# Performance work log

Measured on AMD Instinct MI355X. Metric: run time of the kernel, lower is better.

Reference implementation:

```python
import jax, jax.numpy as jnp
import numpy as np

G, B, T = 8, 32, 1000
I_TOT, H_TOT = 512, 512
Ig, Hg = I_TOT // G, H_TOT // G  # 64, 64


def setup_inputs() -> dict:
    key = jax.random.key(0)
    ks = jax.random.split(key, 6)
    return {
        "x_seq": jax.random.normal(ks[0], (B, T, I_TOT), dtype=jnp.float32),
        "h0": jax.random.normal(ks[1], (G, B, Hg), dtype=jnp.float32),
        # per-group GRU params, TF gate order [z, r, n]
        "W": jax.random.normal(ks[2], (G, Ig, 3 * Hg), dtype=jnp.float32) * 0.1,   # kernel
        "U": jax.random.normal(ks[3], (G, Hg, 3 * Hg), dtype=jnp.float32) * 0.1,   # recurrent kernel
        "b_i": jax.random.normal(ks[4], (G, 3 * Hg), dtype=jnp.float32) * 0.1,     # input bias
        "b_h": jax.random.normal(ks[5], (G, 3 * Hg), dtype=jnp.float32) * 0.1,     # recurrent bias
    }


def _grouped_gru(x_seq, h0, W, U, b_i, b_h):
    b, t, _ = x_seq.shape
    g, ig, _ = W.shape
    hg = U.shape[1]
    # [B,T,I] -> [T,G,B,Ig]
    x = x_seq.reshape(b, t, g, ig).transpose(1, 2, 0, 3)

    def step(h, x_t):
        # h: [G,B,Hg], x_t: [G,B,Ig]
        gx = jnp.einsum('gbi,gij->gbj', x_t, W) + b_i[:, None, :]  # [G,B,3Hg]
        gh = jnp.einsum('gbh,ghj->gbj', h, U) + b_h[:, None, :]    # [G,B,3Hg]
        xz, xr, xn = jnp.split(gx, 3, axis=-1)
        hz, hr, hn = jnp.split(gh, 3, axis=-1)
        z = jax.nn.sigmoid(xz + hz)
        r = jax.nn.sigmoid(xr + hr)
        n = jnp.tanh(xn + r * hn)  # reset_after=True: reset applied after recurrent matmul
        h_new = z * h + (1.0 - z) * n
        return h_new, h_new

    h_out, ys = jax.lax.scan(step, h0, x)  # ys: [T,G,B,Hg]
    output = ys.transpose(2, 0, 1, 3).reshape(b, t, g * hg)  # [B,T,H]
    return output, h_out


def reference(x_seq, h0, W, U, b_i, b_h):
    return _grouped_gru(x_seq, h0, W, U, b_i, b_h)
```

## Files before the change

### kernel.cpp

```cpp
#include <hip/hip_runtime.h>

#define TS 1000

typedef _Float16 half2v __attribute__((ext_vector_type(2)));

__device__ __forceinline__ float rl(float v, int l) {
    return __int_as_float(__builtin_amdgcn_readlane(__float_as_int(v), l));
}
__device__ __forceinline__ int rli(int v, int l) {
    return __builtin_amdgcn_readlane(v, l);
}
__device__ __forceinline__ float fsig(float x) {
    return __builtin_amdgcn_rcpf(1.0f + __expf(-x));
}
__device__ __forceinline__ float ftanh(float x) {
    return 1.0f - 2.0f * __builtin_amdgcn_rcpf(1.0f + __expf(2.0f * x));
}

__global__ __launch_bounds__(512)
__attribute__((amdgpu_waves_per_eu(2, 2)))
void gru_win(const float* __restrict__ x, const float* __restrict__ h0,
             const float* __restrict__ W, const float* __restrict__ U,
             const float* __restrict__ bi, const float* __restrict__ bh,
             float* __restrict__ out, float* __restrict__ hout)
{
    __shared__ float4 ppart[2][4][4][64];
    __shared__ float4 psum[2][4][64];

    const int tid  = threadIdx.x;
    const int lane = tid & 63;
    const int wid  = tid >> 6;
    const bool cons = (wid == 0);
    const bool prod = (wid == 1) || (wid == 2) || (wid == 3) || (wid == 5);
    const int sw   = (wid == 5) ? 3 : (wid - 1);
    const int kb   = __builtin_amdgcn_readfirstlane(prod ? sw * 16 : 0);

    const int g = blockIdx.x >> 5, b = blockIdx.x & 31;

    int uw[96];
    float h = 0.f, bhz = 0.f, bhr = 0.f, bhn = 0.f;
    float* op = out + (size_t)b * (TS * 512) + g * 64 + lane;
    if (cons) {
        const float* Ug = U + (size_t)g * (64 * 192) + lane;
        #pragma unroll
        for (int k2 = 0; k2 < 32; ++k2) {
            #pragma unroll
            for (int gate = 0; gate < 3; ++gate) {
                const float a = Ug[(2 * k2) * 192 + gate * 64];
                const float c = Ug[(2 * k2 + 1) * 192 + gate * 64];
                half2v p; p.x = (_Float16)a; p.y = (_Float16)c;
                uw[gate * 32 + k2] = __builtin_bit_cast(int, p);
            }
        }
        #pragma unroll
        for (int k2 = 0; k2 < 32; ++k2)
            asm volatile("" : "+v"(uw[k2]), "+v"(uw[32 + k2]), "+v"(uw[64 + k2]));
        bhz = bh[g * 192 + lane];
        bhr = bh[g * 192 + 64 + lane];
        bhn = bh[g * 192 + 128 + lane];
        h   = h0[(g * 32 + b) * 64 + lane];
    }

    float w0[16], w1[16], w2[16];
    float bz = 0.f, br = 0.f, bn = 0.f;
    const float* xp = x + (size_t)b * (TS * 512) + g * 64 + lane;
    float xa0 = 0, xa1 = 0, xa2 = 0, xa3 = 0, xb0 = 0, xb1 = 0, xb2 = 0, xb3 = 0;
    if (prod) {
        const float* Wg = W + (size_t)g * (64 * 192) + (size_t)kb * 192 + lane;
        #pragma unroll
        for (int k = 0; k < 16; ++k) {
            w0[k] = Wg[k * 192];
            w1[k] = Wg[k * 192 + 64];
            w2[k] = Wg[k * 192 + 128];
        }
        #pragma unroll
        for (int k = 0; k < 16; ++k)
            asm volatile("" : "+v"(w0[k]), "+v"(w1[k]), "+v"(w2[k]));
        if (sw == 0) {
            bz = bi[g * 192 + lane];
            br = bi[g * 192 + 64 + lane];
            bn = bi[g * 192 + 128 + lane];
        }
    }

#define XLOAD(DST, T_)                                                        \
    { const float* pp_ = xp + (size_t)(T_) * 512;                             \
      asm volatile("global_load_dword %0, %1, off" : "=v"(DST) : "v"(pp_)); }

#define PPROD(XS, SLOT, J)                                                    \
    {                                                                         \
        float az = bz, ar = br, an = bn, az2 = 0.f, ar2 = 0.f, an2 = 0.f;     \
        _Pragma("unroll")                                                     \
        for (int k = 0; k < 8; ++k) {                                         \
            const float s = rl(XS, kb + k);                                   \
            az = fmaf(s, w0[k], az); ar = fmaf(s, w1[k], ar); an = fmaf(s, w2[k], an); \
        }                                                                     \
        _Pragma("unroll")                                                     \
        for (int k = 8; k < 16; ++k) {                                        \
            const float s = rl(XS, kb + k);                                   \
            az2 = fmaf(s, w0[k], az2); ar2 = fmaf(s, w1[k], ar2); an2 = fmaf(s, w2[k], an2); \
        }                                                                     \
        ppart[SLOT][J][sw][lane] = make_float4(az + az2, ar + ar2, an + an2, 0.f); \
    }

#define PREDUCE(SLOT)                                                         \
    {                                                                         \
        const float4 q0 = ppart[SLOT][sw][0][lane];                           \
        const float4 q1 = ppart[SLOT][sw][1][lane];                           \
        const float4 q2 = ppart[SLOT][sw][2][lane];                           \
        const float4 q3 = ppart[SLOT][sw][3][lane];                           \
        psum[SLOT][sw][lane] = make_float4(((q0.x + q1.x) + q2.x) + q3.x,     \
                                           ((q0.y + q1.y) + q2.y) + q3.y,     \
                                           ((q0.z + q1.z) + q2.z) + q3.z, 0.f); \
    }

#define CSTEP(P, J)                                                           \
    {                                                                         \
        const float4 q = psum[P][J][lane];                                    \
        const int hxi = __builtin_amdgcn_update_dpp(                          \
            0, __float_as_int(h), 0xB1 , 0xF, 0xF, true); \
        half2v hp; hp.x = (_Float16)h; hp.y = (_Float16)__int_as_float(hxi);  \
        const int hpi = __builtin_bit_cast(int, hp);                          \
        float az = bhz, ar = bhr, an = bhn, az2 = 0.f, ar2 = 0.f, an2 = 0.f;  \
        _Pragma("unroll")                                                     \
        for (int k2 = 0; k2 < 16; ++k2) {                                     \
            const half2v hv = __builtin_bit_cast(half2v, rli(hpi, 2 * k2));   \
            az = __builtin_amdgcn_fdot2(__builtin_bit_cast(half2v, uw[k2]),      hv, az, false); \
            ar = __builtin_amdgcn_fdot2(__builtin_bit_cast(half2v, uw[32 + k2]), hv, ar, false); \
            an = __builtin_amdgcn_fdot2(__builtin_bit_cast(half2v, uw[64 + k2]), hv, an, false); \
        }                                                                     \
        _Pragma("unroll")                                                     \
        for (int k2 = 16; k2 < 32; ++k2) {                                    \
            const half2v hv = __builtin_bit_cast(half2v, rli(hpi, 2 * k2));   \
            az2 = __builtin_amdgcn_fdot2(__builtin_bit_cast(half2v, uw[k2]),      hv, az2, false); \
            ar2 = __builtin_amdgcn_fdot2(__builtin_bit_cast(half2v, uw[32 + k2]), hv, ar2, false); \
            an2 = __builtin_amdgcn_fdot2(__builtin_bit_cast(half2v, uw[64 + k2]), hv, an2, false); \
        }                                                                     \
        const float z = fsig(q.x + (az + az2));                               \
        const float r = fsig(q.y + (ar + ar2));                               \
        const float n = ftanh(fmaf(r, (an + an2), q.z));     \
        h = n + z * (h - n);                                                  \
        op[0] = h; op += 512;                                                 \
    }

    if (prod) {
        XLOAD(xa0, 0) XLOAD(xa1, 1) XLOAD(xa2, 2) XLOAD(xa3, 3)
        XLOAD(xb0, 4) XLOAD(xb1, 5) XLOAD(xb2, 6) XLOAD(xb3, 7)
        asm volatile("s_waitcnt vmcnt(0)"
                     : "+v"(xa0), "+v"(xa1), "+v"(xa2), "+v"(xa3),
                       "+v"(xb0), "+v"(xb1), "+v"(xb2), "+v"(xb3));
        PPROD(xa0, 0, 0) PPROD(xa1, 0, 1) PPROD(xa2, 0, 2) PPROD(xa3, 0, 3)
        PPROD(xb0, 1, 0) PPROD(xb1, 1, 1) PPROD(xb2, 1, 2) PPROD(xb3, 1, 3)
        XLOAD(xa0, 8) XLOAD(xa1, 9) XLOAD(xa2, 10) XLOAD(xa3, 11)
    }
    asm volatile("s_waitcnt lgkmcnt(0)" ::: "memory");
    __builtin_amdgcn_s_barrier();
    if (prod) PREDUCE(0)
    asm volatile("s_waitcnt lgkmcnt(0)" ::: "memory");
    __builtin_amdgcn_s_barrier();

#define WINDOW(P, XU0, XU1, XU2, XU3, XF0, XF1, XF2, XF3)                     \
    {                                                                         \
        const int t0 = (dw * 2 + (P)) * 4;                                    \
        if (prod) {                                                           \
            int tl;                                                           \
            tl = t0 + 12; if (tl > TS - 1) tl = TS - 1; XLOAD(XF0, tl)        \
            tl = t0 + 13; if (tl > TS - 1) tl = TS - 1; XLOAD(XF1, tl)        \
            tl = t0 + 14; if (tl > TS - 1) tl = TS - 1; XLOAD(XF2, tl)        \
            tl = t0 + 15; if (tl > TS - 1) tl = TS - 1; XLOAD(XF3, tl)        \
            asm volatile("s_waitcnt vmcnt(4)"                                 \
                         : "+v"(XU0), "+v"(XU1), "+v"(XU2), "+v"(XU3));       \
            PPROD(XU0, P, 0) PPROD(XU1, P, 1) PPROD(XU2, P, 2) PPROD(XU3, P, 3) \
            PREDUCE((P) ^ 1)                                                  \
        }                                                                     \
        if (cons) {                                                           \
            CSTEP(P, 0) CSTEP(P, 1) CSTEP(P, 2) CSTEP(P, 3)                   \
        }                                                                     \
        asm volatile("s_waitcnt lgkmcnt(0)" ::: "memory");                    \
        __builtin_amdgcn_sched_barrier(0);                                    \
        __builtin_amdgcn_s_barrier();                     \
        __builtin_amdgcn_sched_barrier(0);                                    \
    }

    for (int dw = 0; dw < 125; ++dw) {
        WINDOW(0, xa0, xa1, xa2, xa3, xb0, xb1, xb2, xb3)
        WINDOW(1, xb0, xb1, xb2, xb3, xa0, xa1, xa2, xa3)
    }
#undef WINDOW
#undef CSTEP
#undef PREDUCE
#undef PPROD
#undef XLOAD

    if (cons)
        hout[(g * 32 + b) * 64 + lane] = h;
}

extern "C" void kernel_launch(void* const* d_in, const int* in_sizes, int n_in,
                              void* d_out, int out_size, void* d_ws, size_t ws_size,
                              hipStream_t stream) {
    const float* x  = (const float*)d_in[0];
    const float* h0 = (const float*)d_in[1];
    const float* W  = (const float*)d_in[2];
    const float* U  = (const float*)d_in[3];
    const float* bi = (const float*)d_in[4];
    const float* bh = (const float*)d_in[5];
    float* out  = (float*)d_out;
    float* hout = out + (size_t)32 * TS * 512;
    hipLaunchKernelGGL(gru_win, dim3(256), dim3(512), 0, stream,
                       x, h0, W, U, bi, bh, out, hout);
}
```

Measured before the change: 331.7 us.

## Give each producer wave whole timesteps with fp16 dot2 input projection

```diff
diff --git a/kernel.cpp b/kernel.cpp
--- a/kernel.cpp
+++ b/kernel.cpp
@@ -4,9 +4,6 @@
 
 typedef _Float16 half2v __attribute__((ext_vector_type(2)));
 
-__device__ __forceinline__ float rl(float v, int l) {
-    return __int_as_float(__builtin_amdgcn_readlane(__float_as_int(v), l));
-}
 __device__ __forceinline__ int rli(int v, int l) {
     return __builtin_amdgcn_readlane(v, l);
 }
@@ -19,162 +16,123 @@
 
 __global__ __launch_bounds__(512)
 __attribute__((amdgpu_waves_per_eu(2, 2)))
-void gru_win(const float* __restrict__ x, const float* __restrict__ h0,
+void gru_uni(const float* __restrict__ x, const float* __restrict__ h0,
              const float* __restrict__ W, const float* __restrict__ U,
              const float* __restrict__ bi, const float* __restrict__ bh,
              float* __restrict__ out, float* __restrict__ hout)
 {
-    __shared__ float4 ppart[2][4][4][64];
-    __shared__ float4 psum[2][4][64];
+    __shared__ float4 psum[4][4][64];
 
     const int tid  = threadIdx.x;
     const int lane = tid & 63;
     const int wid  = tid >> 6;
     const bool cons = (wid == 0);
-    const bool prod = (wid == 1) || (wid == 2) || (wid == 3) || (wid == 5);
-    const int sw   = (wid == 5) ? 3 : (wid - 1);
-    const int kb   = __builtin_amdgcn_readfirstlane(prod ? sw * 16 : 0);
+    const bool prod = (wid == 1) | (wid == 2) | (wid == 3) | (wid == 5);
+    const int jmap = (wid == 5) ? 3 : (wid - 1);
 
     const int g = blockIdx.x >> 5, b = blockIdx.x & 31;
 
     int uw[96];
-    float h = 0.f, bhz = 0.f, bhr = 0.f, bhn = 0.f;
-    float* op = out + (size_t)b * (TS * 512) + g * 64 + lane;
-    if (cons) {
-        const float* Ug = U + (size_t)g * (64 * 192) + lane;
+    {
+        const float* Pg = (cons ? U : W) + (size_t)g * (64 * 192) + lane;
         #pragma unroll
         for (int k2 = 0; k2 < 32; ++k2) {
             #pragma unroll
             for (int gate = 0; gate < 3; ++gate) {
-                const float a = Ug[(2 * k2) * 192 + gate * 64];
-                const float c = Ug[(2 * k2 + 1) * 192 + gate * 64];
+                const float a = Pg[(2 * k2) * 192 + gate * 64];
+                const float c = Pg[(2 * k2 + 1) * 192 + gate * 64];
                 half2v p; p.x = (_Float16)a; p.y = (_Float16)c;
                 uw[gate * 32 + k2] = __builtin_bit_cast(int, p);
             }
         }
-        #pragma unroll
-        for (int k2 = 0; k2 < 32; ++k2)
-            asm volatile("" : "+v"(uw[k2]), "+v"(uw[32 + k2]), "+v"(uw[64 + k2]));
-        bhz = bh[g * 192 + lane];
-        bhr = bh[g * 192 + 64 + lane];
-        bhn = bh[g * 192 + 128 + lane];
-        h   = h0[(g * 32 + b) * 64 + lane];
+    }
+    #pragma unroll
+    for (int k2 = 0; k2 < 32; ++k2)
+        asm volatile("" : "+v"(uw[k2]), "+v"(uw[32 + k2]), "+v"(uw[64 + k2]));
+
+    float b0 = 0.f, b1 = 0.f, b2 = 0.f;
+    {
+        const float* bb = (cons ? bh : bi) + g * 192 + lane;
+        b0 = bb[0]; b1 = bb[64]; b2 = bb[128];
     }
 
-    float w0[16], w1[16], w2[16];
-    float bz = 0.f, br = 0.f, bn = 0.f;
+    float h = 0.f;
+    if (cons) h = h0[(g * 32 + b) * 64 + lane];
+
     const float* xp = x + (size_t)b * (TS * 512) + g * 64 + lane;
-    float xa0 = 0, xa1 = 0, xa2 = 0, xa3 = 0, xb0 = 0, xb1 = 0, xb2 = 0, xb3 = 0;
-    if (prod) {
-        const float* Wg = W + (size_t)g * (64 * 192) + (size_t)kb * 192 + lane;
-        #pragma unroll
-        for (int k = 0; k < 16; ++k) {
-            w0[k] = Wg[k * 192];
-            w1[k] = Wg[k * 192 + 64];
-            w2[k] = Wg[k * 192 + 128];
-        }
-        #pragma unroll
-        for (int k = 0; k < 16; ++k)
-            asm volatile("" : "+v"(w0[k]), "+v"(w1[k]), "+v"(w2[k]));
-        if (sw == 0) {
-            bz = bi[g * 192 + lane];
-            br = bi[g * 192 + 64 + lane];
-            bn = bi[g * 192 + 128 + lane];
-        }
+    float* op = out + (size_t)b * (TS * 512) + g * 64 + lane;
+
+#define MATVEC(SRCV, OZ, OR, ON)                                              \
+    {                                                                         \
+        const int sxi_ = __builtin_amdgcn_update_dpp(                         \
+            0, __float_as_int(SRCV), 0xB1, 0xF, 0xF, true);                   \
+        half2v sp_; sp_.x = (_Float16)(SRCV);                                 \
+        sp_.y = (_Float16)__int_as_float(sxi_);                               \
+        const int spi_ = __builtin_bit_cast(int, sp_);                        \
+        float _az = b0, _ar = b1, _an = b2, _az2 = 0.f, _ar2 = 0.f, _an2 = 0.f; \
+        _Pragma("unroll")                                                     \
+        for (int k2 = 0; k2 < 16; ++k2) {                                     \
+            const half2v hv_ = __builtin_bit_cast(half2v, rli(spi_, 2 * k2)); \
+            _az = __builtin_amdgcn_fdot2(__builtin_bit_cast(half2v, uw[k2]),      hv_, _az, false); \
+            _ar = __builtin_amdgcn_fdot2(__builtin_bit_cast(half2v, uw[32 + k2]), hv_, _ar, false); \
+            _an = __builtin_amdgcn_fdot2(__builtin_bit_cast(half2v, uw[64 + k2]), hv_, _an, false); \
+        }                                                                     \
+        _Pragma("unroll")                                                     \
+        for (int k2 = 16; k2 < 32; ++k2) {                                    \
+            const half2v hv_ = __builtin_bit_cast(half2v, rli(spi_, 2 * k2)); \
+            _az2 = __builtin_amdgcn_fdot2(__builtin_bit_cast(half2v, uw[k2]),      hv_, _az2, false); \
+            _ar2 = __builtin_amdgcn_fdot2(__builtin_bit_cast(half2v, uw[32 + k2]), hv_, _ar2, false); \
+            _an2 = __builtin_amdgcn_fdot2(__builtin_bit_cast(half2v, uw[64 + k2]), hv_, _an2, false); \
+        }                                                                     \
+        OZ = _az + _az2; OR = _ar + _ar2; ON = _an + _an2;                    \
     }
 
 #define XLOAD(DST, T_)                                                        \
     { const float* pp_ = xp + (size_t)(T_) * 512;                             \
       asm volatile("global_load_dword %0, %1, off" : "=v"(DST) : "v"(pp_)); }
 
-#define PPROD(XS, SLOT, J)                                                    \
+#define PSTEP(XS, WR)                                                         \
     {                                                                         \
-        float az = bz, ar = br, an = bn, az2 = 0.f, ar2 = 0.f, an2 = 0.f;     \
-        _Pragma("unroll")                                                     \
-        for (int k = 0; k < 8; ++k) {                                         \
-            const float s = rl(XS, kb + k);                                   \
-            az = fmaf(s, w0[k], az); ar = fmaf(s, w1[k], ar); an = fmaf(s, w2[k], an); \
-        }                                                                     \
-        _Pragma("unroll")                                                     \
-        for (int k = 8; k < 16; ++k) {                                        \
-            const float s = rl(XS, kb + k);                                   \
-            az2 = fmaf(s, w0[k], az2); ar2 = fmaf(s, w1[k], ar2); an2 = fmaf(s, w2[k], an2); \
-        }                                                                     \
-        ppart[SLOT][J][sw][lane] = make_float4(az + az2, ar + ar2, an + an2, 0.f); \
+        float pz_, pr_, pn_;                                                  \
+        MATVEC(XS, pz_, pr_, pn_)                                             \
+        psum[WR][jmap][lane] = make_float4(pz_, pr_, pn_, 0.f);               \
     }
 
-#define PREDUCE(SLOT)                                                         \
+#define CSTEP(RD, J)                                                          \
     {                                                                         \
-        const float4 q0 = ppart[SLOT][sw][0][lane];                           \
-        const float4 q1 = ppart[SLOT][sw][1][lane];                           \
-        const float4 q2 = ppart[SLOT][sw][2][lane];                           \
-        const float4 q3 = ppart[SLOT][sw][3][lane];                           \
-        psum[SLOT][sw][lane] = make_float4(((q0.x + q1.x) + q2.x) + q3.x,     \
-                                           ((q0.y + q1.y) + q2.y) + q3.y,     \
-                                           ((q0.z + q1.z) + q2.z) + q3.z, 0.f); \
-    }
-
-#define CSTEP(P, J)                                                           \
-    {                                                                         \
-        const float4 q = psum[P][J][lane];                                    \
-        const int hxi = __builtin_amdgcn_update_dpp(                          \
-            0, __float_as_int(h), 0xB1 , 0xF, 0xF, true); \
-        half2v hp; hp.x = (_Float16)h; hp.y = (_Float16)__int_as_float(hxi);  \
-        const int hpi = __builtin_bit_cast(int, hp);                          \
-        float az = bhz, ar = bhr, an = bhn, az2 = 0.f, ar2 = 0.f, an2 = 0.f;  \
-        _Pragma("unroll")                                                     \
-        for (int k2 = 0; k2 < 16; ++k2) {                                     \
-            const half2v hv = __builtin_bit_cast(half2v, rli(hpi, 2 * k2));   \
-            az = __builtin_amdgcn_fdot2(__builtin_bit_cast(half2v, uw[k2]),      hv, az, false); \
-            ar = __builtin_amdgcn_fdot2(__builtin_bit_cast(half2v, uw[32 + k2]), hv, ar, false); \
-            an = __builtin_amdgcn_fdot2(__builtin_bit_cast(half2v, uw[64 + k2]), hv, an, false); \
-        }                                                                     \
-        _Pragma("unroll")                                                     \
-        for (int k2 = 16; k2 < 32; ++k2) {                                    \
-            const half2v hv = __builtin_bit_cast(half2v, rli(hpi, 2 * k2));   \
-            az2 = __builtin_amdgcn_fdot2(__builtin_bit_cast(half2v, uw[k2]),      hv, az2, false); \
-            ar2 = __builtin_amdgcn_fdot2(__builtin_bit_cast(half2v, uw[32 + k2]), hv, ar2, false); \
-            an2 = __builtin_amdgcn_fdot2(__builtin_bit_cast(half2v, uw[64 + k2]), hv, an2, false); \
-        }                                                                     \
-        const float z = fsig(q.x + (az + az2));                               \
-        const float r = fsig(q.y + (ar + ar2));                               \
-        const float n = ftanh(fmaf(r, (an + an2), q.z));     \
+        const float4 q = psum[RD][J][lane];                                   \
+        float ghz, ghr, ghn;                                                  \
+        MATVEC(h, ghz, ghr, ghn)                                              \
+        const float z = fsig(q.x + ghz);                                      \
+        const float r = fsig(q.y + ghr);                                      \
+        const float n = ftanh(fmaf(r, ghn, q.z));            \
         h = n + z * (h - n);                                                  \
         op[0] = h; op += 512;                                                 \
     }
 
+    float xa = 0.f, xb = 0.f;
     if (prod) {
-        XLOAD(xa0, 0) XLOAD(xa1, 1) XLOAD(xa2, 2) XLOAD(xa3, 3)
-        XLOAD(xb0, 4) XLOAD(xb1, 5) XLOAD(xb2, 6) XLOAD(xb3, 7)
-        asm volatile("s_waitcnt vmcnt(0)"
-                     : "+v"(xa0), "+v"(xa1), "+v"(xa2), "+v"(xa3),
-                       "+v"(xb0), "+v"(xb1), "+v"(xb2), "+v"(xb3));
-        PPROD(xa0, 0, 0) PPROD(xa1, 0, 1) PPROD(xa2, 0, 2) PPROD(xa3, 0, 3)
-        PPROD(xb0, 1, 0) PPROD(xb1, 1, 1) PPROD(xb2, 1, 2) PPROD(xb3, 1, 3)
-        XLOAD(xa0, 8) XLOAD(xa1, 9) XLOAD(xa2, 10) XLOAD(xa3, 11)
+        XLOAD(xa, jmap) XLOAD(xb, 4 + jmap)
+        asm volatile("s_waitcnt vmcnt(0)" : "+v"(xa), "+v"(xb));
+        PSTEP(xa, 0)
+        PSTEP(xb, 1)
+        XLOAD(xa, 8 + jmap)
     }
     asm volatile("s_waitcnt lgkmcnt(0)" ::: "memory");
     __builtin_amdgcn_s_barrier();
-    if (prod) PREDUCE(0)
-    asm volatile("s_waitcnt lgkmcnt(0)" ::: "memory");
-    __builtin_amdgcn_s_barrier();
 
-#define WINDOW(P, XU0, XU1, XU2, XU3, XF0, XF1, XF2, XF3)                     \
+#define WINDOW(P, XU, XF)                                                     \
     {                                                                         \
-        const int t0 = (dw * 2 + (P)) * 4;                                    \
-        if (prod) {                                                           \
-            int tl;                                                           \
-            tl = t0 + 12; if (tl > TS - 1) tl = TS - 1; XLOAD(XF0, tl)        \
-            tl = t0 + 13; if (tl > TS - 1) tl = TS - 1; XLOAD(XF1, tl)        \
-            tl = t0 + 14; if (tl > TS - 1) tl = TS - 1; XLOAD(XF2, tl)        \
-            tl = t0 + 15; if (tl > TS - 1) tl = TS - 1; XLOAD(XF3, tl)        \
-            asm volatile("s_waitcnt vmcnt(4)"                                 \
-                         : "+v"(XU0), "+v"(XU1), "+v"(XU2), "+v"(XU3));       \
-            PPROD(XU0, P, 0) PPROD(XU1, P, 1) PPROD(XU2, P, 2) PPROD(XU3, P, 3) \
-            PREDUCE((P) ^ 1)                                                  \
-        }                                                                     \
+        const int w  = dw * 2 + (P);                                          \
+        const int rd = w & 3;                                                 \
+        const int wr = (w + 2) & 3;                                           \
         if (cons) {                                                           \
-            CSTEP(P, 0) CSTEP(P, 1) CSTEP(P, 2) CSTEP(P, 3)                   \
+            CSTEP(rd, 0) CSTEP(rd, 1) CSTEP(rd, 2) CSTEP(rd, 3)               \
+        } else if (prod) {                                                    \
+            int tl = 4 * (w + 3) + jmap; if (tl > TS - 1) tl = TS - 1;        \
+            XLOAD(XF, tl)                                                     \
+            asm volatile("s_waitcnt vmcnt(1)" : "+v"(XU));                    \
+            PSTEP(XU, wr)                                                     \
         }                                                                     \
         asm volatile("s_waitcnt lgkmcnt(0)" ::: "memory");                    \
         __builtin_amdgcn_sched_barrier(0);                                    \
@@ -183,14 +141,14 @@
     }
 
     for (int dw = 0; dw < 125; ++dw) {
-        WINDOW(0, xa0, xa1, xa2, xa3, xb0, xb1, xb2, xb3)
-        WINDOW(1, xb0, xb1, xb2, xb3, xa0, xa1, xa2, xa3)
+        WINDOW(0, xa, xb)
+        WINDOW(1, xb, xa)
     }
 #undef WINDOW
 #undef CSTEP
-#undef PREDUCE
-#undef PPROD
+#undef PSTEP
 #undef XLOAD
+#undef MATVEC
 
     if (cons)
         hout[(g * 32 + b) * 64 + lane] = h;
@@ -207,6 +165,6 @@
     const float* bh = (const float*)d_in[5];
     float* out  = (float*)d_out;
     float* hout = out + (size_t)32 * TS * 512;
-    hipLaunchKernelGGL(gru_win, dim3(256), dim3(512), 0, stream,
+    hipLaunchKernelGGL(gru_uni, dim3(256), dim3(512), 0, stream,
                        x, h0, W, U, bi, bh, out, hout);
 }
```

Result: faster. 318.2 us, median of 2 (-4.1%).
